# Performance work log

Hardware: AMD Instinct MI355X
Metric: run time of the kernel (lower is better)

The kernel has to match this reference:

```python
import jax, jax.numpy as jnp
import numpy as np

B, N, DIM = 2, 2048, 2048
N_HEAD, N_KV_HEAD = 32, 8
HEAD_DIM = DIM // N_HEAD  # 64
NEG_INF = -1e9


def setup_inputs() -> dict:
    key = jax.random.key(0)
    ks = jax.random.split(key, 4)
    x = jax.random.normal(ks[0], (B, N, DIM), dtype=jnp.float32)
    Wq = jax.random.normal(ks[1], (DIM, N_HEAD * HEAD_DIM), dtype=jnp.float32) * (DIM ** -0.5)
    Wkv = jax.random.normal(ks[2], (DIM, 2 * N_KV_HEAD * HEAD_DIM), dtype=jnp.float32) * (DIM ** -0.5)
    Wo = jax.random.normal(ks[3], (N_HEAD * HEAD_DIM, DIM), dtype=jnp.float32) * (DIM ** -0.5)
    # RoPE angles: freqs = 1/theta^(2i/d), angle[p, i] = p * freqs[i]
    freqs = 1.0 / (10000.0 ** (jnp.arange(0, HEAD_DIM, 2, dtype=jnp.float32) / HEAD_DIM))
    angles = jnp.arange(N, dtype=jnp.float32)[:, None] * freqs[None, :]  # (N, HEAD_DIM//2)
    rope_cos = jnp.cos(angles)
    rope_sin = jnp.sin(angles)
    # additive causal mask (n, n)
    mask = jnp.where(jnp.tril(jnp.ones((N, N), dtype=bool)), 0.0, NEG_INF).astype(jnp.float32)
    return {"x": x, "Wq": Wq, "Wkv": Wkv, "Wo": Wo, "rope_cos": rope_cos, "rope_sin": rope_sin, "mask": mask, "start_pos": 0}


def apply_rope(x, cos, sin):
    # x: (b, n, h, d); cos/sin: (n, d//2). Complex mult on interleaved pairs.
    xr = x.reshape(*x.shape[:-1], HEAD_DIM // 2, 2)
    xe, xo = xr[..., 0], xr[..., 1]
    c = cos[None, :, None, :]
    s = sin[None, :, None, :]
    yr = xe * c - xo * s
    yi = xe * s + xo * c
    return jnp.stack([yr, yi], axis=-1).reshape(x.shape)


def reference(x, Wq, Wkv, Wo, rope_cos, rope_sin, mask, start_pos):
    b, n, _ = x.shape
    q = (x @ Wq).reshape(b, n, N_HEAD, HEAD_DIM)
    kv = (x @ Wkv).reshape(b, n, 2, N_KV_HEAD, HEAD_DIM)
    k, v = kv[:, :, 0], kv[:, :, 1]
    q = apply_rope(q, rope_cos, rope_sin)
    k = apply_rope(k, rope_cos, rope_sin)
    # repeat kv heads: 'b n h d -> b n (r h) d'
    r = N_HEAD // N_KV_HEAD
    k = jnp.tile(k, (1, 1, r, 1))
    v = jnp.tile(v, (1, 1, r, 1))
    scale = HEAD_DIM ** -0.5
    attn = jnp.einsum('bnhd,bmhd->bhnm', q, k) * scale + mask[None, None]
    attn = jax.nn.softmax(attn, axis=-1)
    out = jnp.einsum('bhnm,bmhd->bnhd', attn, v).reshape(b, n, N_HEAD * HEAD_DIM)
    return out @ Wo
```

## Files before the change

kernel.cpp:

```cpp
#include <hip/hip_runtime.h>


#define BSZ  2
#define NSEQ 2048
#define DIMD 2048
#define NH   32
#define NKV  8
#define HD   64
#define TK   32

typedef __bf16 bf16x8 __attribute__((ext_vector_type(8)));
typedef __bf16 bf16x4 __attribute__((ext_vector_type(4)));
typedef __bf16 bf16x2 __attribute__((ext_vector_type(2)));
typedef float  floatx4 __attribute__((ext_vector_type(4)));
typedef float  floatx16 __attribute__((ext_vector_type(16)));
typedef unsigned int uintx4 __attribute__((ext_vector_type(4)));

#define MFMA16(a, b, c) __builtin_amdgcn_mfma_f32_16x16x32_bf16(a, b, c, 0, 0, 0)
#define MFMA32(a, b, c) __builtin_amdgcn_mfma_f32_32x32x16_bf16(a, b, c, 0, 0, 0)

#define WAITV(n) asm volatile("s_waitcnt vmcnt(" #n ")" ::: "memory")

__device__ __forceinline__ void barrier_nodrain() {
    asm volatile("" ::: "memory");
    __builtin_amdgcn_sched_barrier(0);
    __builtin_amdgcn_s_barrier();
    __builtin_amdgcn_sched_barrier(0);
    asm volatile("" ::: "memory");
}

__device__ __forceinline__ void gload_lds16(const void* g, void* l) {
    __builtin_amdgcn_global_load_lds((const __attribute__((address_space(1))) void*)g,
                                     (__attribute__((address_space(3))) void*)l, 16, 0, 0);
}

__device__ __forceinline__ unsigned pk2(float a, float b) {
    bf16x2 t; t[0] = (__bf16)a; t[1] = (__bf16)b;
    return __builtin_bit_cast(unsigned, t);
}

__global__ void cvt_x_kernel(const float* __restrict__ in, __bf16* __restrict__ out, int n4) {
    int i = blockIdx.x * blockDim.x + threadIdx.x;
    if (i >= n4) return;
    float4 v = ((const float4*)in)[i];
    bf16x4 o;
    o[0] = (__bf16)v.x; o[1] = (__bf16)v.y; o[2] = (__bf16)v.z; o[3] = (__bf16)v.w;
    ((bf16x4*)out)[i] = o;
}

__global__ void transpose_cvt_kernel(const float* __restrict__ W, __bf16* __restrict__ Wt,
                                     int C, int K) {
    __shared__ float t[32][33];
    int c0 = blockIdx.x * 32, r0 = blockIdx.y * 32;
    int lx = threadIdx.x & 31, ly = threadIdx.x >> 5;
    for (int i = 0; i < 32; i += 8)
        t[ly + i][lx] = W[(size_t)(r0 + ly + i) * C + c0 + lx];
    __syncthreads();
    for (int i = 0; i < 32; i += 8)
        Wt[(size_t)(c0 + ly + i) * K + r0 + lx] = (__bf16)t[lx][ly + i];
}


#define MMAC(mh, nh)                                                           \
    {                                                                          \
        asm volatile("s_waitcnt lgkmcnt(0)" ::: "memory");                     \
        __builtin_amdgcn_sched_barrier(0);                                     \
        __builtin_amdgcn_s_setprio(1);                                         \
        _Pragma("unroll")                                                      \
        for (int il = 0; il < 4; ++il)                                         \
            _Pragma("unroll")                                                  \
            for (int jl = 0; jl < 2; ++jl)                                     \
                _Pragma("unroll")                                              \
                for (int ks = 0; ks < 2; ++ks)                                 \
                    acc[(mh) * 4 + il][(nh) * 2 + jl] =                        \
                        MFMA16(af[il][ks], bfr[jl][ks],                        \
                               acc[(mh) * 4 + il][(nh) * 2 + jl]);             \
        __builtin_amdgcn_s_setprio(0);                                         \
        barrier_nodrain();                                                     \
    }

__device__ __forceinline__ void gemm256_8ph(const __bf16* __restrict__ Ap,
                                            const __bf16* __restrict__ Bp,
                                            __bf16* As, __bf16* Bs,
                                            floatx4 (&acc)[8][4]) {
    int tid = threadIdx.x;
    int wave = tid >> 6, lane = tid & 63;
    int wm = wave >> 2, wn = wave & 3;
    int quad = lane >> 4, l16 = lane & 15;
    int swk = l16 & 7;

    int srcc = ((tid & 7) ^ ((tid >> 3) & 7)) << 3;
    int srow = tid >> 3;
    int wb = wave * 512;

    auto stage = [&](const __bf16* panel, __bf16* region, int kt) {
        gload_lds16(panel + (size_t)srow * DIMD + kt * 64 + srcc, region + wb);
        gload_lds16(panel + (size_t)(64 + srow) * DIMD + kt * 64 + srcc,
                    region + 4096 + wb);
    };

    bf16x8 af[4][2], bfr[2][2];
    auto rdA = [&](const __bf16* R) {
        #pragma unroll
        for (int il = 0; il < 4; ++il) {
            int rl = (2 * il + wm) * 16 + l16;
            #pragma unroll
            for (int ks = 0; ks < 2; ++ks)
                af[il][ks] = *(const bf16x8*)&R[rl * 64 + (((ks * 4 + quad) ^ swk) << 3)];
        }
    };
    auto rdB = [&](const __bf16* R) {
        #pragma unroll
        for (int jl = 0; jl < 2; ++jl) {
            int rl = (4 * jl + wn) * 16 + l16;
            #pragma unroll
            for (int ks = 0; ks < 2; ++ks)
                bfr[jl][ks] = *(const bf16x8*)&R[rl * 64 + (((ks * 4 + quad) ^ swk) << 3)];
        }
    };

    const __bf16* ApH1 = Ap + (size_t)128 * DIMD;
    const __bf16* BpH1 = Bp + (size_t)128 * DIMD;

    stage(Ap,   As + 0,    0);  stage(ApH1, As + 8192, 0);
    stage(Bp,   Bs + 0,    0);  stage(BpH1, Bs + 8192, 0);
    stage(Ap,   As + 16384, 1); stage(BpH1, Bs + 16384 + 8192, 1);

    #pragma unroll 2
    for (int t = 0; t < TK; ++t) {
        int b = t & 1;
        __bf16* Ab  = As + (b << 14);
        __bf16* Bb  = Bs + (b << 14);
        __bf16* Aob = As + ((b ^ 1) << 14);
        __bf16* Bob = Bs + ((b ^ 1) << 14);

        if (t < TK - 1) { WAITV(4); } else { WAITV(0); }
        barrier_nodrain();

        rdA(Ab);
        rdB(Bb);
        if (t + 1 < TK) stage(ApH1, Aob + 8192, t + 1);
        MMAC(0, 0);
        rdB(Bb + 8192);
        if (t + 1 < TK) stage(Bp, Bob, t + 1);
        MMAC(0, 1);
        rdA(Ab + 8192);
        if (t + 2 < TK) stage(Ap, Ab, t + 2);
        MMAC(1, 1);
        rdB(Bb);
        if (t + 2 < TK) stage(BpH1, Bb + 8192, t + 2);
        MMAC(1, 0);
    }
}

#define AROW(i) (((i) >> 2 << 7) + ((2 * ((i) & 3) + wm) << 4) + (quad << 2))
#define BCOL(j) (((j) >> 1 << 7) + ((4 * ((j) & 1) + wn) << 4) + l16)


#define MMAC_O(mh, nh)                                                         \
    {                                                                          \
        asm volatile("s_waitcnt lgkmcnt(0)" ::: "memory");                     \
        __builtin_amdgcn_sched_barrier(0);                                     \
        __builtin_amdgcn_s_setprio(1);                                         \
        _Pragma("unroll")                                                      \
        for (int il = 0; il < 2; ++il)                                         \
            _Pragma("unroll")                                                  \
            for (int jl = 0; jl < 2; ++jl)                                     \
                _Pragma("unroll")                                              \
                for (int ks = 0; ks < 2; ++ks)                                 \
                    acc[(mh) * 2 + il][(nh) * 2 + jl] =                        \
                        MFMA16(af[il][ks], bfr[jl][ks],                        \
                               acc[(mh) * 2 + il][(nh) * 2 + jl]);             \
        __builtin_amdgcn_s_setprio(0);                                         \
        barrier_nodrain();                                                     \
    }

__device__ __forceinline__ void gemm128x256_8ph(const __bf16* __restrict__ Ap,
                                                const __bf16* __restrict__ Bp,
                                                __bf16* As, __bf16* Bs,
                                                floatx4 (&acc)[4][4]) {
    int tid = threadIdx.x;
    int wave = tid >> 6, lane = tid & 63;
    int wm = wave >> 2, wn = wave & 3;
    int quad = lane >> 4, l16 = lane & 15;
    int swk = l16 & 7;

    int srcc = ((tid & 7) ^ ((tid >> 3) & 7)) << 3;
    int srow = tid >> 3;
    int wb = wave * 512;

    auto stageA = [&](const __bf16* panel, __bf16* region, int kt) {
        gload_lds16(panel + (size_t)srow * DIMD + kt * 64 + srcc, region + wb);
    };
    auto stageB = [&](const __bf16* panel, __bf16* region, int kt) {
        gload_lds16(panel + (size_t)srow * DIMD + kt * 64 + srcc, region + wb);
        gload_lds16(panel + (size_t)(64 + srow) * DIMD + kt * 64 + srcc,
                    region + 4096 + wb);
    };

    bf16x8 af[2][2], bfr[2][2];
    auto rdA = [&](const __bf16* R) {
        #pragma unroll
        for (int il = 0; il < 2; ++il) {
            int rl = (2 * il + wm) * 16 + l16;
            #pragma unroll
            for (int ks = 0; ks < 2; ++ks)
                af[il][ks] = *(const bf16x8*)&R[rl * 64 + (((ks * 4 + quad) ^ swk) << 3)];
        }
    };
    auto rdB = [&](const __bf16* R) {
        #pragma unroll
        for (int jl = 0; jl < 2; ++jl) {
            int rl = (4 * jl + wn) * 16 + l16;
            #pragma unroll
            for (int ks = 0; ks < 2; ++ks)
                bfr[jl][ks] = *(const bf16x8*)&R[rl * 64 + (((ks * 4 + quad) ^ swk) << 3)];
        }
    };

    const __bf16* ApH1 = Ap + (size_t)64 * DIMD;
    const __bf16* BpH1 = Bp + (size_t)128 * DIMD;

    stageA(Ap,   As + 0,    0);  stageA(ApH1, As + 4096, 0);
    stageB(Bp,   Bs + 0,    0);  stageB(BpH1, Bs + 8192, 0);
    stageA(Ap,   As + 8192, 1);  stageB(BpH1, Bs + 16384 + 8192, 1);

    #pragma unroll 2
    for (int t = 0; t < TK; ++t) {
        int b = t & 1;
        __bf16* Ab  = As + (b << 13);
        __bf16* Bb  = Bs + (b << 14);
        __bf16* Aob = As + ((b ^ 1) << 13);
        __bf16* Bob = Bs + ((b ^ 1) << 14);

        if (t < TK - 1) { WAITV(3); } else { WAITV(0); }
        barrier_nodrain();

        rdA(Ab);
        rdB(Bb);
        if (t + 1 < TK) stageA(ApH1, Aob + 4096, t + 1);
        MMAC_O(0, 0);
        rdB(Bb + 8192);
        if (t + 1 < TK) stageB(Bp, Bob, t + 1);
        MMAC_O(0, 1);
        rdA(Ab + 4096);
        if (t + 2 < TK) stageA(Ap, Ab, t + 2);
        MMAC_O(1, 1);
        rdB(Bb);
        if (t + 2 < TK) stageB(BpH1, Bb + 8192, t + 2);
        MMAC_O(1, 0);
    }
}

#define AROW128(i) (((i) >> 1) * 64 + ((2 * ((i) & 1) + wm) << 4) + (quad << 2))

__global__ __launch_bounds__(512, 2) void gemm_qkv_kernel(
    const __bf16* __restrict__ A, const __bf16* __restrict__ Bt,
    const float* __restrict__ cosb, const float* __restrict__ sinb,
    __bf16* __restrict__ Qo, __bf16* __restrict__ Ko, __bf16* __restrict__ Vo) {
    __shared__ __align__(16) __bf16 As[2 * 2 * 8192];
    __shared__ __align__(16) __bf16 Bs[2 * 2 * 8192];
    int p0 = blockIdx.x * 256;
    int t0 = blockIdx.y * 256;

    floatx4 acc[8][4] = {};
    gemm256_8ph(Bt + (size_t)p0 * DIMD, A + (size_t)t0 * DIMD, As, Bs, acc);

    int tid = threadIdx.x;
    int wave = tid >> 6, lane = tid & 63;
    int wm = wave >> 2, wn = wave & 3;
    int quad = lane >> 4, l16 = lane & 15;
    bool isQ = p0 < 2048;
    bool isV = p0 >= 2560;
    const float sc = isQ ? 0.18033688f : 1.0f;

    #pragma unroll
    for (int i = 0; i < 8; ++i) {
        int pp = p0 + AROW(i);
        int dq = pp & 63;
        #pragma unroll
        for (int j = 0; j < 4; ++j) {
            int t = t0 + BCOL(j);
            int b = t >> 11, n = t & 2047;
            float x0 = acc[i][j][0], x1 = acc[i][j][1];
            float x2 = acc[i][j][2], x3 = acc[i][j][3];
            if (!isV) {
                int d2 = dq >> 1;
                float2 cv = *(const float2*)(cosb + (size_t)n * 32 + d2);
                float2 sv = *(const float2*)(sinb + (size_t)n * 32 + d2);
                bf16x4 o;
                o[0] = (__bf16)((x0 * cv.x - x1 * sv.x) * sc);
                o[1] = (__bf16)((x0 * sv.x + x1 * cv.x) * sc);
                o[2] = (__bf16)((x2 * cv.y - x3 * sv.y) * sc);
                o[3] = (__bf16)((x2 * sv.y + x3 * cv.y) * sc);
                if (isQ) {
                    int h = pp >> 6;
                    *(bf16x4*)&Qo[((size_t)(b * NH + h) * NSEQ + n) * HD + dq] = o;
                } else {
                    int kvh = (pp - 2048) >> 6;
                    *(bf16x4*)&Ko[((size_t)(b * NKV + kvh) * NSEQ + n) * HD + dq] = o;
                }
            } else {
                int kvh = (pp - 2560) >> 6;
                size_t base = (size_t)(b * NKV + kvh) * HD;
                Vo[(base + dq + 0) * NSEQ + n] = (__bf16)x0;
                Vo[(base + dq + 1) * NSEQ + n] = (__bf16)x1;
                Vo[(base + dq + 2) * NSEQ + n] = (__bf16)x2;
                Vo[(base + dq + 3) * NSEQ + n] = (__bf16)x3;
            }
        }
    }
}

__global__ __launch_bounds__(512, 2) void gemm_out_kernel(
    const __bf16* __restrict__ A, const __bf16* __restrict__ Bt,
    float* __restrict__ C) {
    __shared__ __align__(16) __bf16 As[2 * 8192];
    __shared__ __align__(16) __bf16 Bs[2 * 2 * 8192];
    int n0 = blockIdx.x * 256;
    int m0 = blockIdx.y * 128;

    floatx4 acc[4][4] = {};
    gemm128x256_8ph(A + (size_t)m0 * DIMD, Bt + (size_t)n0 * DIMD, As, Bs, acc);

    int tid = threadIdx.x;
    int wave = tid >> 6, lane = tid & 63;
    int wm = wave >> 2, wn = wave & 3;
    int quad = lane >> 4, l16 = lane & 15;
    #pragma unroll
    for (int i = 0; i < 4; ++i) {
        int row = m0 + AROW128(i);
        #pragma unroll
        for (int j = 0; j < 4; ++j) {
            int col = n0 + BCOL(j);
            float* Cp = C + (size_t)row * 2048 + col;
            Cp[0]    = acc[i][j][0];
            Cp[2048] = acc[i][j][1];
            Cp[4096] = acc[i][j][2];
            Cp[6144] = acc[i][j][3];
        }
    }
}

__global__ __launch_bounds__(256) void attn_kernel(
    const __bf16* __restrict__ Q, const __bf16* __restrict__ K,
    const __bf16* __restrict__ Vt, __bf16* __restrict__ O) {
    __shared__ __align__(16) __bf16 Kl[2][64 * 64];
    __shared__ __align__(16) __bf16 Vl[2][64 * 64];

    int tid = threadIdx.x;
    int wave = tid >> 6, lane = tid & 63;
    int l31 = lane & 31, hi = lane >> 5;
    int bk = blockIdx.x;
    int b = bk >> 3, kvh = bk & 7;
    int h = kvh + 8 * wave;
    int y = blockIdx.y;

    const __bf16* Qbase = Q + ((size_t)(b * NH + h)) * NSEQ * HD;
    const __bf16* Kbase = K + ((size_t)(b * NKV + kvh)) * NSEQ * HD;
    const __bf16* Vbase = Vt + ((size_t)(b * NKV + kvh)) * HD * NSEQ;
    int swl = (l31 & 7) << 3;

    auto stage = [&](int kt, int bi) {
        #pragma unroll
        for (int r = 0; r < 2; ++r) {
            int obase = r * 2048 + wave * 512;
            int o = obase + lane * 8;
            int row = o >> 6;
            int el = (o & 63) ^ ((row & 7) << 3);
            gload_lds16(Kbase + (size_t)kt * 4096 + row * 64 + el, &Kl[bi][obase]);
            gload_lds16(Vbase + (size_t)row * NSEQ + kt * 64 + el, &Vl[bi][obase]);
        }
    };

    int pb = 0;
    stage(0, 0);

    for (int ph = 0; ph < 2; ++ph) {
        int qt = ph ? y : 63 - y;
        int q0 = qt * 32;
        int J = (q0 + 31) >> 6;
        int par = qt & 1;

        bf16x8 qf[4];
        #pragma unroll
        for (int t = 0; t < 4; ++t)
            qf[t] = *(const bf16x8*)(Qbase + (size_t)(q0 + l31) * HD + t * 16 + hi * 8);

        floatx16 oacc[2] = {};
        float lsum = 0.0f;

        for (int kt = 0; kt <= J; ++kt) {
            __syncthreads();
            if (kt < J) stage(kt + 1, pb ^ 1);
            else if (ph == 0) stage(0, pb ^ 1);
            const __bf16* Kp = &Kl[pb][0];
            const __bf16* Vp = &Vl[pb][0];
            bool diag = (kt == J);

            #pragma unroll
            for (int kvt = 0; kvt < 2; ++kvt) {
                if (diag && !par && kvt == 1) continue;
                bool domask = diag && (kvt == par);

                floatx16 s = {};
                #pragma unroll
                for (int t = 0; t < 4; ++t) {
                    bf16x8 ka = *(const bf16x8*)&Kp[(kvt * 32 + l31) * 64 +
                                                    ((t * 16 + hi * 8) ^ swl)];
                    s = MFMA32(ka, qf[t], s);
                }

                #pragma unroll
                for (int ks = 0; ks < 2; ++ks) {
                    float e[8];
                    if (domask) {
                        int q_l = q0 + l31;
                        #pragma unroll
                        for (int r = 0; r < 8; ++r) {
                            int kv = kt * 64 + kvt * 32 + ks * 16 +
                                     (r & 3) + 8 * (r >> 2) + 4 * hi;
                            float p = __builtin_exp2f(s[ks * 8 + r]);
                            e[r] = (kv > q_l) ? 0.0f : p;
                        }
                    } else {
                        #pragma unroll
                        for (int r = 0; r < 8; ++r)
                            e[r] = __builtin_exp2f(s[ks * 8 + r]);
                    }
                    #pragma unroll
                    for (int r = 0; r < 8; ++r) lsum += e[r];

                    unsigned a0 = pk2(e[0], e[1]), a1 = pk2(e[2], e[3]);
                    unsigned b0 = pk2(e[4], e[5]), b1 = pk2(e[6], e[7]);
                    unsigned t0 = hi ? a0 : b0, t1 = hi ? a1 : b1;
                    unsigned s0 = (unsigned)__shfl_xor((int)t0, 32, 64);
                    unsigned s1 = (unsigned)__shfl_xor((int)t1, 32, 64);
                    uintx4 fw;
                    fw[0] = hi ? s0 : a0;
                    fw[1] = hi ? s1 : a1;
                    fw[2] = hi ? b0 : s0;
                    fw[3] = hi ? b1 : s1;
                    bf16x8 pfrag = __builtin_bit_cast(bf16x8, fw);

                    #pragma unroll
                    for (int dt = 0; dt < 2; ++dt) {
                        bf16x8 va = *(const bf16x8*)&Vp[(dt * 32 + l31) * 64 +
                                        ((kvt * 32 + ks * 16 + hi * 8) ^ swl)];
                        oacc[dt] = MFMA32(va, pfrag, oacc[dt]);
                    }
                }
            }
            pb ^= 1;
        }

        lsum += __shfl_xor(lsum, 32, 64);
        float inv = 1.0f / lsum;
        __bf16* Op = O + ((size_t)(b * NSEQ + q0 + l31)) * (NH * HD) + h * HD;
        #pragma unroll
        for (int dt = 0; dt < 2; ++dt)
            #pragma unroll
            for (int g = 0; g < 4; ++g) {
                bf16x4 ov;
                #pragma unroll
                for (int r = 0; r < 4; ++r) ov[r] = (__bf16)(oacc[dt][4 * g + r] * inv);
                *(bf16x4*)(Op + dt * 32 + 8 * g + 4 * hi) = ov;
            }
    }
}

extern "C" void kernel_launch(void* const* d_in, const int* in_sizes, int n_in,
                              void* d_out, int out_size, void* d_ws, size_t ws_size,
                              hipStream_t stream) {
    const float* x   = (const float*)d_in[0];
    const float* Wq  = (const float*)d_in[1];
    const float* Wkv = (const float*)d_in[2];
    const float* Wo  = (const float*)d_in[3];
    const float* rc  = (const float*)d_in[4];
    const float* rs  = (const float*)d_in[5];
    float* out = (float*)d_out;
    char* ws = (char*)d_ws;

    __bf16* xb    = (__bf16*)(ws + 0);
    __bf16* wqkvt = (__bf16*)(ws + 16777216);
    __bf16* wot   = (__bf16*)(ws + 29360128);
    __bf16* Qb    = (__bf16*)(ws + 37748736);
    __bf16* Kb    = (__bf16*)(ws + 54525952);
    __bf16* Vtb   = (__bf16*)(ws + 58720256);
    __bf16* attnb = (__bf16*)(ws + 62914560);

    cvt_x_kernel<<<8192, 256, 0, stream>>>(x, xb, 2097152);
    transpose_cvt_kernel<<<dim3(64, 64), 256, 0, stream>>>(Wq, wqkvt, 2048, 2048);
    transpose_cvt_kernel<<<dim3(32, 64), 256, 0, stream>>>(Wkv, wqkvt + (size_t)2048 * 2048, 1024, 2048);
    transpose_cvt_kernel<<<dim3(64, 64), 256, 0, stream>>>(Wo, wot, 2048, 2048);

    gemm_qkv_kernel<<<dim3(12, 16), 512, 0, stream>>>(xb, wqkvt, rc, rs, Qb, Kb, Vtb);

    attn_kernel<<<dim3(16, 32), 256, 0, stream>>>(Qb, Kb, Vtb, attnb);

    gemm_out_kernel<<<dim3(8, 32), 512, 0, stream>>>(attnb, wot, out);
}
```

Measured before the change: 322.7 us.

## Drop LDS staging in attention, one query tile per block; fuse prep kernels

The attention kernel no longer double-buffers K/V tiles through LDS. Each block now handles a single 32-row query tile, with 64 blocks in y instead of 32 paired tiles, and reads K and V fragments straight from global memory in 32-key steps. This removes the barriers and LDS traffic but loses sharing of K/V across the four waves and the causal load balancing that pairing gave. The four convert/transpose launches are also merged into one prep kernel to save launch overhead.

```diff
diff --git a/kernel.cpp b/kernel.cpp
--- a/kernel.cpp
+++ b/kernel.cpp
@@ -39,25 +39,41 @@
     return __builtin_bit_cast(unsigned, t);
 }
 
-__global__ void cvt_x_kernel(const float* __restrict__ in, __bf16* __restrict__ out, int n4) {
-    int i = blockIdx.x * blockDim.x + threadIdx.x;
-    if (i >= n4) return;
-    float4 v = ((const float4*)in)[i];
-    bf16x4 o;
-    o[0] = (__bf16)v.x; o[1] = (__bf16)v.y; o[2] = (__bf16)v.z; o[3] = (__bf16)v.w;
-    ((bf16x4*)out)[i] = o;
-}
-
-__global__ void transpose_cvt_kernel(const float* __restrict__ W, __bf16* __restrict__ Wt,
-                                     int C, int K) {
-    __shared__ float t[32][33];
-    int c0 = blockIdx.x * 32, r0 = blockIdx.y * 32;
+__device__ __forceinline__ void transpose32(const float* __restrict__ W,
+                                            __bf16* __restrict__ Wt,
+                                            int C, int K, int bx, int by,
+                                            float (*t)[33]) {
+    int c0 = bx * 32, r0 = by * 32;
     int lx = threadIdx.x & 31, ly = threadIdx.x >> 5;
     for (int i = 0; i < 32; i += 8)
         t[ly + i][lx] = W[(size_t)(r0 + ly + i) * C + c0 + lx];
     __syncthreads();
     for (int i = 0; i < 32; i += 8)
         Wt[(size_t)(c0 + ly + i) * K + r0 + lx] = (__bf16)t[lx][ly + i];
+}
+
+__global__ void prep_kernel(const float* __restrict__ x, __bf16* __restrict__ xb,
+                            const float* __restrict__ Wq, const float* __restrict__ Wkv,
+                            const float* __restrict__ Wo,
+                            __bf16* __restrict__ wqkvt, __bf16* __restrict__ wot) {
+    __shared__ float t[32][33];
+    int blk = blockIdx.x;
+    if (blk < 8192) {
+        int i = blk * 256 + threadIdx.x;
+        float4 v = ((const float4*)x)[i];
+        bf16x4 o;
+        o[0] = (__bf16)v.x; o[1] = (__bf16)v.y; o[2] = (__bf16)v.z; o[3] = (__bf16)v.w;
+        ((bf16x4*)xb)[i] = o;
+    } else if (blk < 12288) {
+        int q = blk - 8192;
+        transpose32(Wq, wqkvt, 2048, 2048, q & 63, q >> 6, t);
+    } else if (blk < 14336) {
+        int q = blk - 12288;
+        transpose32(Wkv, wqkvt + (size_t)2048 * 2048, 1024, 2048, q & 31, q >> 5, t);
+    } else {
+        int q = blk - 14336;
+        transpose32(Wo, wot, 2048, 2048, q & 63, q >> 6, t);
+    }
 }
 
 
@@ -345,128 +361,91 @@
 __global__ __launch_bounds__(256) void attn_kernel(
     const __bf16* __restrict__ Q, const __bf16* __restrict__ K,
     const __bf16* __restrict__ Vt, __bf16* __restrict__ O) {
-    __shared__ __align__(16) __bf16 Kl[2][64 * 64];
-    __shared__ __align__(16) __bf16 Vl[2][64 * 64];
-
     int tid = threadIdx.x;
     int wave = tid >> 6, lane = tid & 63;
     int l31 = lane & 31, hi = lane >> 5;
     int bk = blockIdx.x;
     int b = bk >> 3, kvh = bk & 7;
     int h = kvh + 8 * wave;
-    int y = blockIdx.y;
+    int qt = 63 - (int)blockIdx.y;
+    int q0 = qt * 32;
 
     const __bf16* Qbase = Q + ((size_t)(b * NH + h)) * NSEQ * HD;
     const __bf16* Kbase = K + ((size_t)(b * NKV + kvh)) * NSEQ * HD;
     const __bf16* Vbase = Vt + ((size_t)(b * NKV + kvh)) * HD * NSEQ;
-    int swl = (l31 & 7) << 3;
-
-    auto stage = [&](int kt, int bi) {
-        #pragma unroll
-        for (int r = 0; r < 2; ++r) {
-            int obase = r * 2048 + wave * 512;
-            int o = obase + lane * 8;
-            int row = o >> 6;
-            int el = (o & 63) ^ ((row & 7) << 3);
-            gload_lds16(Kbase + (size_t)kt * 4096 + row * 64 + el, &Kl[bi][obase]);
-            gload_lds16(Vbase + (size_t)row * NSEQ + kt * 64 + el, &Vl[bi][obase]);
-        }
-    };
-
-    int pb = 0;
-    stage(0, 0);
-
-    for (int ph = 0; ph < 2; ++ph) {
-        int qt = ph ? y : 63 - y;
-        int q0 = qt * 32;
-        int J = (q0 + 31) >> 6;
-        int par = qt & 1;
-
-        bf16x8 qf[4];
-        #pragma unroll
-        for (int t = 0; t < 4; ++t)
-            qf[t] = *(const bf16x8*)(Qbase + (size_t)(q0 + l31) * HD + t * 16 + hi * 8);
-
-        floatx16 oacc[2] = {};
-        float lsum = 0.0f;
-
-        for (int kt = 0; kt <= J; ++kt) {
-            __syncthreads();
-            if (kt < J) stage(kt + 1, pb ^ 1);
-            else if (ph == 0) stage(0, pb ^ 1);
-            const __bf16* Kp = &Kl[pb][0];
-            const __bf16* Vp = &Vl[pb][0];
-            bool diag = (kt == J);
-
-            #pragma unroll
-            for (int kvt = 0; kvt < 2; ++kvt) {
-                if (diag && !par && kvt == 1) continue;
-                bool domask = diag && (kvt == par);
-
-                floatx16 s = {};
+
+    bf16x8 qf[4];
+    #pragma unroll
+    for (int t = 0; t < 4; ++t)
+        qf[t] = *(const bf16x8*)(Qbase + (size_t)(q0 + l31) * HD + t * 16 + hi * 8);
+
+    floatx16 oacc[2] = {};
+    float lsum = 0.0f;
+    int q_l = q0 + l31;
+
+    for (int s = 0; s <= qt; ++s) {
+        int kv0 = s * 32;
+        const __bf16* Krow = Kbase + (size_t)(kv0 + l31) * HD + hi * 8;
+
+        floatx16 sv = {};
+        #pragma unroll
+        for (int t = 0; t < 4; ++t) {
+            bf16x8 ka = *(const bf16x8*)(Krow + t * 16);
+            sv = MFMA32(ka, qf[t], sv);
+        }
+
+        bool diag = (s == qt);
+        #pragma unroll
+        for (int ks = 0; ks < 2; ++ks) {
+            float e[8];
+            if (diag) {
                 #pragma unroll
-                for (int t = 0; t < 4; ++t) {
-                    bf16x8 ka = *(const bf16x8*)&Kp[(kvt * 32 + l31) * 64 +
-                                                    ((t * 16 + hi * 8) ^ swl)];
-                    s = MFMA32(ka, qf[t], s);
+                for (int r = 0; r < 8; ++r) {
+                    int kv = kv0 + ks * 16 + (r & 3) + 8 * (r >> 2) + 4 * hi;
+                    float p = __builtin_exp2f(sv[ks * 8 + r]);
+                    e[r] = (kv > q_l) ? 0.0f : p;
                 }
-
+            } else {
                 #pragma unroll
-                for (int ks = 0; ks < 2; ++ks) {
-                    float e[8];
-                    if (domask) {
-                        int q_l = q0 + l31;
-                        #pragma unroll
-                        for (int r = 0; r < 8; ++r) {
-                            int kv = kt * 64 + kvt * 32 + ks * 16 +
-                                     (r & 3) + 8 * (r >> 2) + 4 * hi;
-                            float p = __builtin_exp2f(s[ks * 8 + r]);
-                            e[r] = (kv > q_l) ? 0.0f : p;
-                        }
-                    } else {
-                        #pragma unroll
-                        for (int r = 0; r < 8; ++r)
-                            e[r] = __builtin_exp2f(s[ks * 8 + r]);
-                    }
-                    #pragma unroll
-                    for (int r = 0; r < 8; ++r) lsum += e[r];
-
-                    unsigned a0 = pk2(e[0], e[1]), a1 = pk2(e[2], e[3]);
-                    unsigned b0 = pk2(e[4], e[5]), b1 = pk2(e[6], e[7]);
-                    unsigned t0 = hi ? a0 : b0, t1 = hi ? a1 : b1;
-                    unsigned s0 = (unsigned)__shfl_xor((int)t0, 32, 64);
-                    unsigned s1 = (unsigned)__shfl_xor((int)t1, 32, 64);
-                    uintx4 fw;
-                    fw[0] = hi ? s0 : a0;
-                    fw[1] = hi ? s1 : a1;
-                    fw[2] = hi ? b0 : s0;
-                    fw[3] = hi ? b1 : s1;
-                    bf16x8 pfrag = __builtin_bit_cast(bf16x8, fw);
-
-                    #pragma unroll
-                    for (int dt = 0; dt < 2; ++dt) {
-                        bf16x8 va = *(const bf16x8*)&Vp[(dt * 32 + l31) * 64 +
-                                        ((kvt * 32 + ks * 16 + hi * 8) ^ swl)];
-                        oacc[dt] = MFMA32(va, pfrag, oacc[dt]);
-                    }
-                }
+                for (int r = 0; r < 8; ++r)
+                    e[r] = __builtin_exp2f(sv[ks * 8 + r]);
             }
-            pb ^= 1;
-        }
-
-        lsum += __shfl_xor(lsum, 32, 64);
-        float inv = 1.0f / lsum;
-        __bf16* Op = O + ((size_t)(b * NSEQ + q0 + l31)) * (NH * HD) + h * HD;
-        #pragma unroll
-        for (int dt = 0; dt < 2; ++dt)
-            #pragma unroll
-            for (int g = 0; g < 4; ++g) {
-                bf16x4 ov;
-                #pragma unroll
-                for (int r = 0; r < 4; ++r) ov[r] = (__bf16)(oacc[dt][4 * g + r] * inv);
-                *(bf16x4*)(Op + dt * 32 + 8 * g + 4 * hi) = ov;
+            #pragma unroll
+            for (int r = 0; r < 8; ++r) lsum += e[r];
+
+            unsigned a0 = pk2(e[0], e[1]), a1 = pk2(e[2], e[3]);
+            unsigned b0 = pk2(e[4], e[5]), b1 = pk2(e[6], e[7]);
+            unsigned t0 = hi ? a0 : b0, t1 = hi ? a1 : b1;
+            unsigned s0 = (unsigned)__shfl_xor((int)t0, 32, 64);
+            unsigned s1 = (unsigned)__shfl_xor((int)t1, 32, 64);
+            uintx4 fw;
+            fw[0] = hi ? s0 : a0;
+            fw[1] = hi ? s1 : a1;
+            fw[2] = hi ? b0 : s0;
+            fw[3] = hi ? b1 : s1;
+            bf16x8 pfrag = __builtin_bit_cast(bf16x8, fw);
+
+            #pragma unroll
+            for (int dt = 0; dt < 2; ++dt) {
+                bf16x8 va = *(const bf16x8*)(Vbase + (size_t)(dt * 32 + l31) * NSEQ +
+                                             kv0 + ks * 16 + hi * 8);
+                oacc[dt] = MFMA32(va, pfrag, oacc[dt]);
             }
-    }
+        }
+    }
+
+    lsum += __shfl_xor(lsum, 32, 64);
+    float inv = 1.0f / lsum;
+    __bf16* Op = O + ((size_t)(b * NSEQ + q0 + l31)) * (NH * HD) + h * HD;
+    #pragma unroll
+    for (int dt = 0; dt < 2; ++dt)
+        #pragma unroll
+        for (int g = 0; g < 4; ++g) {
+            bf16x4 ov;
+            #pragma unroll
+            for (int r = 0; r < 4; ++r) ov[r] = (__bf16)(oacc[dt][4 * g + r] * inv);
+            *(bf16x4*)(Op + dt * 32 + 8 * g + 4 * hi) = ov;
+        }
 }
 
 extern "C" void kernel_launch(void* const* d_in, const int* in_sizes, int n_in,
@@ -489,14 +468,11 @@
     __bf16* Vtb   = (__bf16*)(ws + 58720256);
     __bf16* attnb = (__bf16*)(ws + 62914560);
 
-    cvt_x_kernel<<<8192, 256, 0, stream>>>(x, xb, 2097152);
-    transpose_cvt_kernel<<<dim3(64, 64), 256, 0, stream>>>(Wq, wqkvt, 2048, 2048);
-    transpose_cvt_kernel<<<dim3(32, 64), 256, 0, stream>>>(Wkv, wqkvt + (size_t)2048 * 2048, 1024, 2048);
-    transpose_cvt_kernel<<<dim3(64, 64), 256, 0, stream>>>(Wo, wot, 2048, 2048);
+    prep_kernel<<<18432, 256, 0, stream>>>(x, xb, Wq, Wkv, Wo, wqkvt, wot);
 
     gemm_qkv_kernel<<<dim3(12, 16), 512, 0, stream>>>(xb, wqkvt, rc, rs, Qb, Kb, Vtb);
 
-    attn_kernel<<<dim3(16, 32), 256, 0, stream>>>(Qb, Kb, Vtb, attnb);
+    attn_kernel<<<dim3(16, 64), 256, 0, stream>>>(Qb, Kb, Vtb, attnb);
 
     gemm_out_kernel<<<dim3(8, 32), 512, 0, stream>>>(attnb, wot, out);
 }
```

Result: slower. 380.2 us (+17.8%).
